# Performance work log

Hardware: AMD Instinct MI355X
Metric: run time of the kernel (lower is better)

Reference implementation:

```python
import jax, jax.numpy as jnp
import numpy as np

S = 7; B = 2; C = 20; N = 8; BS = 16384
LAMBDA_COORD = 5.0; LAMBDA_NOOBJ = 0.5
EPS = 1e-6


def setup_inputs() -> dict:
    key = jax.random.key(0)
    k1, k2, k3 = jax.random.split(key, 3)
    outputs = jax.random.uniform(k1, (BS, S, S, B * 5 + C), dtype=jnp.float32)
    gt_boxes = jax.random.uniform(k2, (BS, N, 4), dtype=jnp.float32)
    gt_labels = jax.random.randint(k3, (BS, N), 0, C)
    return {"outputs": outputs, "gt_boxes": gt_boxes, "gt_labels": gt_labels}


def _pairwise_iou(pred_xywh, gt_boxes):
    # pred_xywh: [bs,S,S,B,4] (center x,y,w,h); gt_boxes: [bs,N,4] -> iou [bs,S,S,B,N]
    p = pred_xywh[..., None, :]                       # [bs,S,S,B,1,4]
    g = gt_boxes[:, None, None, None, :, :]           # [bs,1,1,1,N,4]
    px1, py1 = p[..., 0] - p[..., 2] / 2, p[..., 1] - p[..., 3] / 2
    px2, py2 = p[..., 0] + p[..., 2] / 2, p[..., 1] + p[..., 3] / 2
    gx1, gy1 = g[..., 0] - g[..., 2] / 2, g[..., 1] - g[..., 3] / 2
    gx2, gy2 = g[..., 0] + g[..., 2] / 2, g[..., 1] + g[..., 3] / 2
    iw = jnp.clip(jnp.minimum(px2, gx2) - jnp.maximum(px1, gx1), 0.0)
    ih = jnp.clip(jnp.minimum(py2, gy2) - jnp.maximum(py1, gy1), 0.0)
    inter = iw * ih
    union = p[..., 2] * p[..., 3] + g[..., 2] * g[..., 3] - inter
    return inter / (union + EPS)


def reference(outputs, gt_boxes, gt_labels):
    bs = outputs.shape[0]
    pred = outputs[..., : B * 5].reshape(bs, S, S, B, 5)   # [bs,S,S,B,5]
    pred_xywh, pred_conf = pred[..., :4], pred[..., 4]
    pred_cls = outputs[..., B * 5:]                        # [bs,S,S,C]

    iou = _pairwise_iou(pred_xywh, gt_boxes)               # [bs,S,S,B,N]

    # Original loop: for each gt j, if iou(:,j).max() > best -> best_iou, best_box_idx = argmax over B.
    iou_max_over_b = jnp.max(iou, axis=3)                  # [bs,S,S,N]
    j_star = jnp.argmax(iou_max_over_b, axis=-1)
    best_iou = jnp.max(iou_max_over_b, axis=-1)            # [bs,S,S]
    iou_at_j = jnp.take_along_axis(iou, j_star[..., None, None], axis=4)[..., 0]  # [bs,S,S,B]
    best_b = jnp.argmax(iou_at_j, axis=-1)                 # [bs,S,S] in [0,B)

    # Faithful to source: gt_boxes indexed by best_box_idx (the pred-box index), requires N >= B.
    gt_sel = jnp.take_along_axis(
        jnp.broadcast_to(gt_boxes[:, None, None], (bs, S, S, N, 4)),
        best_b[..., None, None], axis=3)[..., 0, :]        # [bs,S,S,4]
    pred_sel = jnp.take_along_axis(pred, best_b[..., None, None], axis=3)[..., 0, :]  # [bs,S,S,5]

    loc = ((pred_sel[..., 0] - gt_sel[..., 0]) ** 2
           + (pred_sel[..., 1] - gt_sel[..., 1]) ** 2
           + (jnp.sqrt(pred_sel[..., 2]) - jnp.sqrt(gt_sel[..., 2])) ** 2
           + (jnp.sqrt(pred_sel[..., 3]) - jnp.sqrt(gt_sel[..., 3])) ** 2)
    loc = LAMBDA_COORD * loc                               # [bs,S,S]

    conf_obj = (pred_sel[..., 4] - best_iou) ** 2          # [bs,S,S]

    # Classification: mean cross-entropy of the cell's class logits vs all gt labels
    logp = jax.nn.log_softmax(pred_cls, axis=-1)           # [bs,S,S,C]
    lab = jnp.broadcast_to(gt_labels[:, None, None, :], (bs, S, S, N))
    ce = -jnp.mean(jnp.take_along_axis(logp, lab, axis=3), axis=-1)  # [bs,S,S]

    noobj = LAMBDA_NOOBJ * jnp.sum(pred_conf ** 2, axis=-1)  # [bs,S,S]

    has_obj = best_iou > 0.0
    per_cell = jnp.where(has_obj, loc + conf_obj + ce, noobj)
    return jnp.sum(per_cell) / bs
```

## Files before the change

### kernel.cpp

```cpp
#include <hip/hip_runtime.h>

namespace {

constexpr int kS = 7;
constexpr int kB = 2;
constexpr int kC = 20;
constexpr int kN = 8;
constexpr int kBS = 16384;
constexpr int kCells = kBS * kS * kS;
constexpr int kBlocks = kCells / 256;
constexpr int kF = kB * 5 + kC;
constexpr float kLambdaCoord = 5.0f;
constexpr float kLambdaNoobj = 0.5f;
constexpr float kEps = 1e-6f;

__global__ __launch_bounds__(256) void yolo_loss_kernel(
    const float* __restrict__ outputs,
    const float* __restrict__ gt_boxes,
    const int* __restrict__ gt_labels,
    float* __restrict__ partials) {
  __shared__ float lds[256 * kF];

  const int tid = threadIdx.x;
  const int c0 = blockIdx.x * 256;
  const int bs = (c0 + tid) / (kS * kS);

  float g[kN][4];
  const float4* gb4 = reinterpret_cast<const float4*>(gt_boxes + (size_t)bs * kN * 4);
#pragma unroll
  for (int n = 0; n < kN; ++n) {
    float4 v = gb4[n];
    g[n][0] = v.x; g[n][1] = v.y; g[n][2] = v.z; g[n][3] = v.w;
  }
  const int4* lb4 = reinterpret_cast<const int4*>(gt_labels + (size_t)bs * kN);
  const int4 lab0 = lb4[0];
  const int4 lab1 = lb4[1];

  {
    const float4* src = reinterpret_cast<const float4*>(outputs + (size_t)c0 * kF);
    float4* dst = reinterpret_cast<float4*>(lds);
#pragma unroll
    for (int i = tid; i < 1920; i += 256) dst[i] = src[i];
  }
  __syncthreads();

  const float* x = lds + tid * kF;

  float iou[kB][kN];
#pragma unroll
  for (int b = 0; b < kB; ++b) {
    const float px = x[b * 5 + 0], py = x[b * 5 + 1];
    const float pw = x[b * 5 + 2], ph = x[b * 5 + 3];
    const float px1 = px - pw * 0.5f, px2 = px + pw * 0.5f;
    const float py1 = py - ph * 0.5f, py2 = py + ph * 0.5f;
    const float parea = pw * ph;
#pragma unroll
    for (int n = 0; n < kN; ++n) {
      const float gx = g[n][0], gy = g[n][1], gw = g[n][2], gh = g[n][3];
      const float gx1 = gx - gw * 0.5f, gx2 = gx + gw * 0.5f;
      const float gy1 = gy - gh * 0.5f, gy2 = gy + gh * 0.5f;
      const float iw = fmaxf(fminf(px2, gx2) - fmaxf(px1, gx1), 0.0f);
      const float ih = fmaxf(fminf(py2, gy2) - fmaxf(py1, gy1), 0.0f);
      const float inter = iw * ih;
      const float uni = parea + gw * gh - inter;
      iou[b][n] = inter / (uni + kEps);
    }
  }

  float best_iou = -1.0f;
  float i0j = 0.0f, i1j = 0.0f;
#pragma unroll
  for (int n = 0; n < kN; ++n) {
    const float m = fmaxf(iou[0][n], iou[1][n]);
    if (m > best_iou) {
      best_iou = m;
      i0j = iou[0][n];
      i1j = iou[1][n];
    }
  }
  const int bb = (i1j > i0j) ? 1 : 0;

  const float gsx = bb ? g[1][0] : g[0][0];
  const float gsy = bb ? g[1][1] : g[0][1];
  const float gsw = bb ? g[1][2] : g[0][2];
  const float gsh = bb ? g[1][3] : g[0][3];
  const float psx = bb ? x[5] : x[0];
  const float psy = bb ? x[6] : x[1];
  const float psw = bb ? x[7] : x[2];
  const float psh = bb ? x[8] : x[3];
  const float psc = bb ? x[9] : x[4];

  const float dx = psx - gsx;
  const float dy = psy - gsy;
  const float dw = sqrtf(psw) - sqrtf(gsw);
  const float dh = sqrtf(psh) - sqrtf(gsh);
  const float loc = kLambdaCoord * (dx * dx + dy * dy + dw * dw + dh * dh);
  const float conf_obj = (psc - best_iou) * (psc - best_iou);

  float mx = x[10];
#pragma unroll
  for (int k = 1; k < kC; ++k) mx = fmaxf(mx, x[10 + k]);
  float se = 0.0f;
#pragma unroll
  for (int k = 0; k < kC; ++k) se += __expf(x[10 + k] - mx);
  const float lse = mx + __logf(se);

  float ce = 0.0f;
  ce += x[10 + lab0.x] + x[10 + lab0.y] + x[10 + lab0.z] + x[10 + lab0.w];
  ce += x[10 + lab1.x] + x[10 + lab1.y] + x[10 + lab1.z] + x[10 + lab1.w];
  ce = -(ce - 8.0f * lse) * (1.0f / kN);

  const float noobj = kLambdaNoobj * (x[4] * x[4] + x[9] * x[9]);

  float val = (best_iou > 0.0f) ? (loc + conf_obj + ce) : noobj;

#pragma unroll
  for (int off = 32; off > 0; off >>= 1) val += __shfl_down(val, off, 64);
  __shared__ float ws[4];
  const int lane = tid & 63;
  const int wid = tid >> 6;
  if (lane == 0) ws[wid] = val;
  __syncthreads();
  if (tid == 0) {
    partials[blockIdx.x] = ws[0] + ws[1] + ws[2] + ws[3];
  }
}

__global__ __launch_bounds__(256) void reduce_kernel(
    const float* __restrict__ partials, float* __restrict__ out) {
  float s = 0.0f;
  for (int i = threadIdx.x; i < kBlocks; i += 256) s += partials[i];
#pragma unroll
  for (int off = 32; off > 0; off >>= 1) s += __shfl_down(s, off, 64);
  __shared__ float ws[4];
  const int lane = threadIdx.x & 63;
  const int wid = threadIdx.x >> 6;
  if (lane == 0) ws[wid] = s;
  __syncthreads();
  if (threadIdx.x == 0) {
    out[0] = (ws[0] + ws[1] + ws[2] + ws[3]) * (1.0f / kBS);
  }
}

}

extern "C" void kernel_launch(void* const* d_in, const int* in_sizes, int n_in,
                              void* d_out, int out_size, void* d_ws, size_t ws_size,
                              hipStream_t stream) {
  const float* outputs = (const float*)d_in[0];
  const float* gt_boxes = (const float*)d_in[1];
  const int* gt_labels = (const int*)d_in[2];
  float* out = (float*)d_out;
  float* partials = (float*)d_ws;

  yolo_loss_kernel<<<kBlocks, 256, 0, stream>>>(outputs, gt_boxes, gt_labels, partials);
  reduce_kernel<<<1, 256, 0, stream>>>(partials, out);
}
```

Before: 29.86 us.

## Persistent grid with double-buffered direct global-to-LDS tile prefetch

Replaces the one-block-per-tile launch (3136 blocks) with a persistent grid of 512 blocks that loop over tiles. Each next tile is staged into a second LDS buffer with global_load_lds DMA while the current tile is computed, using explicit vmcnt waits and barriers. This aims to overlap memory latency with compute and cut per-block launch and partial-sum overhead. The cost is twice the LDS per block, which lowers occupancy, plus fragile hand-written waitcnt logic: the gt box and label loads inside the loop also count toward vmcnt, so the wait threshold may be wrong.

```diff
diff --git a/kernel.cpp b/kernel.cpp
--- a/kernel.cpp
+++ b/kernel.cpp
@@ -3,133 +3,166 @@
 namespace {
 
 constexpr int kS = 7;
-constexpr int kB = 2;
 constexpr int kC = 20;
 constexpr int kN = 8;
 constexpr int kBS = 16384;
 constexpr int kCells = kBS * kS * kS;
-constexpr int kBlocks = kCells / 256;
-constexpr int kF = kB * 5 + kC;
+constexpr int kF = 30;
+constexpr int kTile = 256;
+constexpr int kNT = kCells / kTile;
+constexpr int kGrid = 512;
 constexpr float kLambdaCoord = 5.0f;
 constexpr float kLambdaNoobj = 0.5f;
 constexpr float kEps = 1e-6f;
+
+typedef const __attribute__((address_space(1))) unsigned int gu32;
+typedef __attribute__((address_space(3))) unsigned int lu32;
+
+__device__ __forceinline__ void stage_tile(const float4* __restrict__ src4,
+                                           float* dst, int tid) {
+  float4* d4 = reinterpret_cast<float4*>(dst);
+#pragma unroll
+  for (int k = 0; k < 7; ++k) {
+    __builtin_amdgcn_global_load_lds((gu32*)(src4 + k * 256 + tid),
+                                     (lu32*)(d4 + k * 256 + tid), 16, 0, 0);
+  }
+  if (tid < 128) {
+    __builtin_amdgcn_global_load_lds((gu32*)(src4 + 1792 + tid),
+                                     (lu32*)(d4 + 1792 + tid), 16, 0, 0);
+  }
+}
 
 __global__ __launch_bounds__(256) void yolo_loss_kernel(
     const float* __restrict__ outputs,
     const float* __restrict__ gt_boxes,
     const int* __restrict__ gt_labels,
     float* __restrict__ partials) {
-  __shared__ float lds[256 * kF];
+  __shared__ float lds[2][kTile * kF];
+  __shared__ float ws[4];
 
   const int tid = threadIdx.x;
-  const int c0 = blockIdx.x * 256;
-  const int bs = (c0 + tid) / (kS * kS);
+  float val = 0.0f;
 
-  float g[kN][4];
-  const float4* gb4 = reinterpret_cast<const float4*>(gt_boxes + (size_t)bs * kN * 4);
+  int t = blockIdx.x;
+  int cur = 0;
+  stage_tile(reinterpret_cast<const float4*>(outputs + (size_t)t * kTile * kF),
+             lds[0], tid);
+
+  while (true) {
+    const int nxt = t + kGrid;
+    if (nxt < kNT) {
+      stage_tile(reinterpret_cast<const float4*>(outputs + (size_t)nxt * kTile * kF),
+                 lds[cur ^ 1], tid);
+      asm volatile("s_waitcnt vmcnt(7)" ::: "memory");
+    } else {
+      asm volatile("s_waitcnt vmcnt(0)" ::: "memory");
+    }
+    __builtin_amdgcn_s_barrier();
+    asm volatile("" ::: "memory");
+
+    {
+      const int c = t * kTile + tid;
+      const int bs = c / (kS * kS);
+      const float* x = &lds[cur][tid * kF];
+
+      float g[kN][4];
+      const float4* gb4 =
+          reinterpret_cast<const float4*>(gt_boxes + (size_t)bs * kN * 4);
 #pragma unroll
-  for (int n = 0; n < kN; ++n) {
-    float4 v = gb4[n];
-    g[n][0] = v.x; g[n][1] = v.y; g[n][2] = v.z; g[n][3] = v.w;
+      for (int n = 0; n < kN; ++n) {
+        float4 v = gb4[n];
+        g[n][0] = v.x; g[n][1] = v.y; g[n][2] = v.z; g[n][3] = v.w;
+      }
+      const int4* lb4 = reinterpret_cast<const int4*>(gt_labels + (size_t)bs * kN);
+      const int4 lab0 = lb4[0];
+      const int4 lab1 = lb4[1];
+
+      float iou[2][kN];
+#pragma unroll
+      for (int b = 0; b < 2; ++b) {
+        const float px = x[b * 5 + 0], py = x[b * 5 + 1];
+        const float pw = x[b * 5 + 2], ph = x[b * 5 + 3];
+        const float px1 = px - pw * 0.5f, px2 = px + pw * 0.5f;
+        const float py1 = py - ph * 0.5f, py2 = py + ph * 0.5f;
+        const float parea = pw * ph;
+#pragma unroll
+        for (int n = 0; n < kN; ++n) {
+          const float gx = g[n][0], gy = g[n][1], gw = g[n][2], gh = g[n][3];
+          const float iw =
+              fmaxf(fminf(px2, gx + gw * 0.5f) - fmaxf(px1, gx - gw * 0.5f), 0.0f);
+          const float ih =
+              fmaxf(fminf(py2, gy + gh * 0.5f) - fmaxf(py1, gy - gh * 0.5f), 0.0f);
+          const float inter = iw * ih;
+          const float uni = parea + gw * gh - inter;
+          iou[b][n] = inter / (uni + kEps);
+        }
+      }
+
+      float best_iou = -1.0f;
+      float i0j = 0.0f, i1j = 0.0f;
+#pragma unroll
+      for (int n = 0; n < kN; ++n) {
+        const float m = fmaxf(iou[0][n], iou[1][n]);
+        if (m > best_iou) { best_iou = m; i0j = iou[0][n]; i1j = iou[1][n]; }
+      }
+      const int bb = (i1j > i0j) ? 1 : 0;
+
+      const float gsx = bb ? g[1][0] : g[0][0];
+      const float gsy = bb ? g[1][1] : g[0][1];
+      const float gsw = bb ? g[1][2] : g[0][2];
+      const float gsh = bb ? g[1][3] : g[0][3];
+      const float psx = bb ? x[5] : x[0];
+      const float psy = bb ? x[6] : x[1];
+      const float psw = bb ? x[7] : x[2];
+      const float psh = bb ? x[8] : x[3];
+      const float psc = bb ? x[9] : x[4];
+
+      const float dx = psx - gsx;
+      const float dy = psy - gsy;
+      const float dw = sqrtf(psw) - sqrtf(gsw);
+      const float dh = sqrtf(psh) - sqrtf(gsh);
+      const float loc = kLambdaCoord * (dx * dx + dy * dy + dw * dw + dh * dh);
+      const float conf_obj = (psc - best_iou) * (psc - best_iou);
+
+      float mx = x[10];
+#pragma unroll
+      for (int k = 1; k < kC; ++k) mx = fmaxf(mx, x[10 + k]);
+      float se = 0.0f;
+#pragma unroll
+      for (int k = 0; k < kC; ++k) se += __expf(x[10 + k] - mx);
+      const float lse = mx + __logf(se);
+
+      float ce = 0.0f;
+      ce += x[10 + lab0.x] + x[10 + lab0.y] + x[10 + lab0.z] + x[10 + lab0.w];
+      ce += x[10 + lab1.x] + x[10 + lab1.y] + x[10 + lab1.z] + x[10 + lab1.w];
+      ce = -(ce - 8.0f * lse) * (1.0f / kN);
+
+      const float noobj = kLambdaNoobj * (x[4] * x[4] + x[9] * x[9]);
+
+      val += (best_iou > 0.0f) ? (loc + conf_obj + ce) : noobj;
+    }
+
+    asm volatile("" ::: "memory");
+    __builtin_amdgcn_s_barrier();
+    if (nxt >= kNT) break;
+    t = nxt;
+    cur ^= 1;
   }
-  const int4* lb4 = reinterpret_cast<const int4*>(gt_labels + (size_t)bs * kN);
-  const int4 lab0 = lb4[0];
-  const int4 lab1 = lb4[1];
-
-  {
-    const float4* src = reinterpret_cast<const float4*>(outputs + (size_t)c0 * kF);
-    float4* dst = reinterpret_cast<float4*>(lds);
-#pragma unroll
-    for (int i = tid; i < 1920; i += 256) dst[i] = src[i];
-  }
-  __syncthreads();
-
-  const float* x = lds + tid * kF;
-
-  float iou[kB][kN];
-#pragma unroll
-  for (int b = 0; b < kB; ++b) {
-    const float px = x[b * 5 + 0], py = x[b * 5 + 1];
-    const float pw = x[b * 5 + 2], ph = x[b * 5 + 3];
-    const float px1 = px - pw * 0.5f, px2 = px + pw * 0.5f;
-    const float py1 = py - ph * 0.5f, py2 = py + ph * 0.5f;
-    const float parea = pw * ph;
-#pragma unroll
-    for (int n = 0; n < kN; ++n) {
-      const float gx = g[n][0], gy = g[n][1], gw = g[n][2], gh = g[n][3];
-      const float gx1 = gx - gw * 0.5f, gx2 = gx + gw * 0.5f;
-      const float gy1 = gy - gh * 0.5f, gy2 = gy + gh * 0.5f;
-      const float iw = fmaxf(fminf(px2, gx2) - fmaxf(px1, gx1), 0.0f);
-      const float ih = fmaxf(fminf(py2, gy2) - fmaxf(py1, gy1), 0.0f);
-      const float inter = iw * ih;
-      const float uni = parea + gw * gh - inter;
-      iou[b][n] = inter / (uni + kEps);
-    }
-  }
-
-  float best_iou = -1.0f;
-  float i0j = 0.0f, i1j = 0.0f;
-#pragma unroll
-  for (int n = 0; n < kN; ++n) {
-    const float m = fmaxf(iou[0][n], iou[1][n]);
-    if (m > best_iou) {
-      best_iou = m;
-      i0j = iou[0][n];
-      i1j = iou[1][n];
-    }
-  }
-  const int bb = (i1j > i0j) ? 1 : 0;
-
-  const float gsx = bb ? g[1][0] : g[0][0];
-  const float gsy = bb ? g[1][1] : g[0][1];
-  const float gsw = bb ? g[1][2] : g[0][2];
-  const float gsh = bb ? g[1][3] : g[0][3];
-  const float psx = bb ? x[5] : x[0];
-  const float psy = bb ? x[6] : x[1];
-  const float psw = bb ? x[7] : x[2];
-  const float psh = bb ? x[8] : x[3];
-  const float psc = bb ? x[9] : x[4];
-
-  const float dx = psx - gsx;
-  const float dy = psy - gsy;
-  const float dw = sqrtf(psw) - sqrtf(gsw);
-  const float dh = sqrtf(psh) - sqrtf(gsh);
-  const float loc = kLambdaCoord * (dx * dx + dy * dy + dw * dw + dh * dh);
-  const float conf_obj = (psc - best_iou) * (psc - best_iou);
-
-  float mx = x[10];
-#pragma unroll
-  for (int k = 1; k < kC; ++k) mx = fmaxf(mx, x[10 + k]);
-  float se = 0.0f;
-#pragma unroll
-  for (int k = 0; k < kC; ++k) se += __expf(x[10 + k] - mx);
-  const float lse = mx + __logf(se);
-
-  float ce = 0.0f;
-  ce += x[10 + lab0.x] + x[10 + lab0.y] + x[10 + lab0.z] + x[10 + lab0.w];
-  ce += x[10 + lab1.x] + x[10 + lab1.y] + x[10 + lab1.z] + x[10 + lab1.w];
-  ce = -(ce - 8.0f * lse) * (1.0f / kN);
-
-  const float noobj = kLambdaNoobj * (x[4] * x[4] + x[9] * x[9]);
-
-  float val = (best_iou > 0.0f) ? (loc + conf_obj + ce) : noobj;
 
 #pragma unroll
   for (int off = 32; off > 0; off >>= 1) val += __shfl_down(val, off, 64);
-  __shared__ float ws[4];
   const int lane = tid & 63;
   const int wid = tid >> 6;
   if (lane == 0) ws[wid] = val;
   __syncthreads();
-  if (tid == 0) {
-    partials[blockIdx.x] = ws[0] + ws[1] + ws[2] + ws[3];
-  }
+  if (tid == 0) partials[blockIdx.x] = ws[0] + ws[1] + ws[2] + ws[3];
 }
 
 __global__ __launch_bounds__(256) void reduce_kernel(
     const float* __restrict__ partials, float* __restrict__ out) {
   float s = 0.0f;
-  for (int i = threadIdx.x; i < kBlocks; i += 256) s += partials[i];
+#pragma unroll
+  for (int i = threadIdx.x; i < kGrid; i += 256) s += partials[i];
 #pragma unroll
   for (int off = 32; off > 0; off >>= 1) s += __shfl_down(s, off, 64);
   __shared__ float ws[4];
@@ -153,6 +186,6 @@
   float* out = (float*)d_out;
   float* partials = (float*)d_ws;
 
-  yolo_loss_kernel<<<kBlocks, 256, 0, stream>>>(outputs, gt_boxes, gt_labels, partials);
+  yolo_loss_kernel<<<kGrid, kTile, 0, stream>>>(outputs, gt_boxes, gt_labels, partials);
   reduce_kernel<<<1, 256, 0, stream>>>(partials, out);
 }
```

Result: slower. 34.02 us (+14.0%).
